# Performance work log

Hardware: AMD Instinct MI355X
Metric: run time of the kernel (lower is better)

## Reference

```python
import jax, jax.numpy as jnp
import numpy as np


def lstm_cell(x, h, c, Wi, Wh, b):
    # PyTorch LSTMCell gate order: i, f, g, o
    g = x @ Wi.T + h @ Wh.T + b
    i, f, gg, o = jnp.split(g, 4, axis=-1)
    c = jax.nn.sigmoid(f) * c + jax.nn.sigmoid(i) * jnp.tanh(gg)
    h = jax.nn.sigmoid(o) * jnp.tanh(c)
    return h, c


def setup_inputs() -> dict:
    key = jax.random.key(0)
    ks = jax.random.split(key, 32)
    S, B, L, N, T = 20, 16, 30, 6, 20
    H, E, Vs, Vt = 512, 512, 50000, 30000
    w = lambda k, shape: jax.random.normal(k, shape, jnp.float32) * 0.05
    return {
        'articles': jax.random.randint(ks[0], (S, B, L), 0, Vs, jnp.int32),
        'summaries': jax.random.randint(ks[1], (N, B, T), 0, Vt, jnp.int32),
        'emb_src': w(ks[2], (Vs, E)),
        'emb_tgt': w(ks[3], (Vt, E)),
        'we_Wi': w(ks[4], (4 * H, E)), 'we_Wh': w(ks[5], (4 * H, H)), 'we_b': w(ks[6], (4 * H,)),
        'se_Wi': w(ks[7], (4 * H, H)), 'se_Wh': w(ks[8], (4 * H, H)), 'se_b': w(ks[9], (4 * H,)),
        'W_feat': w(ks[10], (H, H)), 'b_feat': w(ks[11], (H,)),
        'wd_Wi': w(ks[12], (4 * H, E)), 'wd_Wh': w(ks[13], (4 * H, H)), 'wd_b': w(ks[14], (4 * H,)),
        'W_vocab': w(ks[15], (Vt, H)), 'b_vocab': w(ks[16], (Vt,)),
        'sd_Wi': w(ks[17], (4 * H, H)), 'sd_Wh': w(ks[18], (4 * H, H)), 'sd_b': w(ks[19], (4 * H,)),
        'attn_Wh': w(ks[20], (H, H)), 'attn_wc': w(ks[21], (H,)), 'attn_v': w(ks[22], (H,)),
        'W_out': w(ks[23], (H, 2 * H)), 'b_out': w(ks[24], (H,)),
    }


def _forward(articles, summaries, emb_src, emb_tgt, we_Wi, we_Wh, we_b,
             se_Wi, se_Wh, se_b, W_feat, b_feat, wd_Wi, wd_Wh, wd_b,
             W_vocab, b_vocab, sd_Wi, sd_Wh, sd_b, attn_Wh, attn_wc, attn_v,
             W_out, b_out):
    S, B, L = articles.shape
    H = we_Wh.shape[1]

    # ---- word encoder: LSTMCell over each sentence, vmapped over S ----
    def encode_sentence(tokens):  # [B, L]
        x = emb_src[tokens]  # [B, L, E]
        z = jnp.zeros((B, H), x.dtype)
        def step(hc, xt):
            h, c = lstm_cell(xt, hc[0], hc[1], we_Wi, we_Wh, we_b)
            return (h, c), None
        (h, _), _ = jax.lax.scan(step, (z, z), jnp.swapaxes(x, 0, 1))
        return h
    word_hx = jax.vmap(encode_sentence)(articles)  # [S, B, H]

    # ---- sentence encoder: LSTM over sentence dim ----
    z = jnp.zeros((B, H), word_hx.dtype)
    def senc_step(hc, x):
        h, c = lstm_cell(x, hc[0], hc[1], se_Wi, se_Wh, se_b)
        return (h, c), h
    (s_hx, s_cx), sent_out = jax.lax.scan(senc_step, (z, z), word_hx)  # sent_out [S,B,H]
    sent_feat = sent_out @ W_feat.T + b_feat  # precomputed attention features

    mask = (articles[:, :, 0:1] > 0).astype(jnp.float32)  # [S, B, 1]
    coverage0 = jnp.zeros_like(mask)

    # ---- hierarchical decoder over summary sentences ----
    def sent_step(carry, sent):  # sent [B, T]
        w_hx, w_cx, s_hx, s_cx, coverage, loss = carry
        seq = sent.T  # [T, B]

        def word_step(wc, ba):
            wh, wcell, l = wc
            wb, wa = ba
            wh, wcell = lstm_cell(emb_tgt[wb], wh, wcell, wd_Wi, wd_Wh, wd_b)
            logits = wh @ W_vocab.T + b_vocab  # [B, V]
            logp = jax.nn.log_softmax(logits, axis=-1)
            nll = -jnp.take_along_axis(logp, wa[:, None], axis=1)[:, 0]
            m = (wa != 0).astype(logits.dtype)  # ignore_index=0
            l = l + jnp.sum(nll * m) / jnp.maximum(jnp.sum(m), 1.0)
            return (wh, wcell, l), None

        (w_hx, w_cx, loss), _ = jax.lax.scan(word_step, (w_hx, w_cx, loss), (seq[:-1], seq[1:]))

        # sentence decoder step with coverage attention over S sentences
        s_h2, s_cx = lstm_cell(w_hx, s_hx, s_cx, sd_Wi, sd_Wh, sd_b)
        e = jnp.einsum('sbh,h->sb', jnp.tanh(sent_feat + s_h2 @ attn_Wh.T + coverage * attn_wc), attn_v)
        e = jnp.where(mask[:, :, 0] > 0, e, -1e9)
        align = jax.nn.softmax(e, axis=0)[:, :, None]  # [S, B, 1]
        context = jnp.sum(align * sent_out, axis=0)  # [B, H]
        final = jnp.tanh(jnp.concatenate([context, s_h2], axis=-1) @ W_out.T + b_out)
        # coverage loss (with pre-update coverage), then accumulate coverage
        loss = loss + jnp.mean(jnp.sum(jnp.minimum(align[:, :, 0], coverage[:, :, 0]), axis=0))
        coverage = coverage + align
        return (final, w_cx, final, s_cx, coverage, loss), None

    init = (s_hx, s_cx, s_hx, s_cx, coverage0, jnp.float32(0.0))
    (_, _, _, _, _, loss), _ = jax.lax.scan(sent_step, init, summaries)
    return loss


def reference(articles, summaries, emb_src, emb_tgt, we_Wi, we_Wh, we_b,
              se_Wi, se_Wh, se_b, W_feat, b_feat, wd_Wi, wd_Wh, wd_b,
              W_vocab, b_vocab, sd_Wi, sd_Wh, sd_b, attn_Wh, attn_wc, attn_v,
              W_out, b_out):
    return _forward(articles, summaries, emb_src, emb_tgt, we_Wi, we_Wh, we_b,
                    se_Wi, se_Wh, se_b, W_feat, b_feat, wd_Wi, wd_Wh, wd_b,
                    W_vocab, b_vocab, sd_Wi, sd_Wh, sd_b, attn_Wh, attn_wc,
                    attn_v, W_out, b_out)
```

## Files before the change

kernel.cpp:

```cpp
#include <hip/hip_runtime.h>
#include <cstdint>
#include <cstddef>

#define H 512
#define SS 20
#define BB 16
#define LL 30
#define NN 6
#define TT 20
#define VT 30000
#define MROWS 1824
#define NSTEPS 114
#define MPAD 1856
#define NT2 120
#define VBLK 232
#define UBLK 16

typedef __attribute__((ext_vector_type(8))) short bf16x8;
typedef __attribute__((ext_vector_type(4))) float f32x4;

__device__ __forceinline__ float sigmoidf_(float x) { return 1.f / (1.f + expf(-x)); }
__device__ __forceinline__ float b2f(ushort u) { return __uint_as_float(((uint32_t)u) << 16); }
__device__ __forceinline__ ushort f2b_rne(float f) {
  uint32_t u = __float_as_uint(f);
  return (ushort)((u + 0x7fffu + ((u >> 16) & 1u)) >> 16);
}

__device__ __forceinline__ void gbar(uint* cnt, uint* gen, uint nblk)
{
  __syncthreads();
  if (threadIdx.x == 0) {
    uint g = __hip_atomic_load(gen, __ATOMIC_RELAXED, __HIP_MEMORY_SCOPE_AGENT);
    uint v = __hip_atomic_fetch_add(cnt, 1u, __ATOMIC_ACQ_REL, __HIP_MEMORY_SCOPE_AGENT);
    if (v == nblk - 1u) {
      __hip_atomic_store(cnt, 0u, __ATOMIC_RELAXED, __HIP_MEMORY_SCOPE_AGENT);
      __hip_atomic_store(gen, g + 1u, __ATOMIC_RELEASE, __HIP_MEMORY_SCOPE_AGENT);
    } else {
      while (__hip_atomic_load(gen, __ATOMIC_ACQUIRE, __HIP_MEMORY_SCOPE_AGENT) == g)
        __builtin_amdgcn_s_sleep(2);
    }
  }
  __syncthreads();
}

struct PrepP {
  const int* articles; const int* summaries;
  const float* emb_src; const float* emb_tgt;
  const float* we_Wi; const float* wd_Wi; const float* we_Wh;
  const float* se_Wi; const float* se_Wh; const float* W_feat;
  const float* wd_Wh; const float* sd_Wi; const float* sd_Wh;
  const float* attn_Wh; const float* W_out;
  ushort* A_we; ushort* A_wd;
  ushort* weWi; ushort* wdWi; ushort* weWh;
  ushort* seWi; ushort* seWh; ushort* wfeat;
  ushort* wdWh; ushort* sdWi; ushort* sdWh;
  ushort* attnWh; ushort* Wout;
};

__device__ __forceinline__ void conv_f2b(const float* __restrict__ src,
                                         ushort* __restrict__ dst, int n4,
                                         int t0, int stride)
{
  for (int i = t0; i < n4; i += stride) {
    float4 v = reinterpret_cast<const float4*>(src)[i];
    ushort4 o;
    o.x = f2b_rne(v.x); o.y = f2b_rne(v.y);
    o.z = f2b_rne(v.z); o.w = f2b_rne(v.w);
    reinterpret_cast<ushort4*>(dst)[i] = o;
  }
}

__global__ __launch_bounds__(256) void prep_kernel(PrepP P)
{
  const int t0 = blockIdx.x * 256 + threadIdx.x;
  const int stride = gridDim.x * 256;
  for (int i = t0; i < SS * BB * LL * H; i += stride) {
    int m = i >> 9, k = i & 511;
    int l = m / (SS * BB), sb = m % (SS * BB);
    int tok = P.articles[sb * LL + l];
    P.A_we[i] = f2b_rne(P.emb_src[(size_t)tok * H + k]);
  }
  for (int i = t0; i < MROWS * H; i += stride) {
    int m = i >> 9, k = i & 511;
    int stp = m >> 4, b = m & 15;
    int n = stp / (TT - 1), t = stp % (TT - 1);
    int tok = P.summaries[(n * BB + b) * TT + t];
    P.A_wd[i] = f2b_rne(P.emb_tgt[(size_t)tok * H + k]);
  }
  const int Q = 4 * H * H / 4;
  conv_f2b(P.we_Wi, P.weWi, Q, t0, stride);
  conv_f2b(P.wd_Wi, P.wdWi, Q, t0, stride);
  conv_f2b(P.we_Wh, P.weWh, Q, t0, stride);
  conv_f2b(P.se_Wi, P.seWi, Q, t0, stride);
  conv_f2b(P.se_Wh, P.seWh, Q, t0, stride);
  conv_f2b(P.wd_Wh, P.wdWh, Q, t0, stride);
  conv_f2b(P.sd_Wi, P.sdWi, Q, t0, stride);
  conv_f2b(P.sd_Wh, P.sdWh, Q, t0, stride);
  conv_f2b(P.W_feat, P.wfeat, H * H / 4, t0, stride);
  conv_f2b(P.attn_Wh, P.attnWh, H * H / 4, t0, stride);
  conv_f2b(P.W_out, P.Wout, H * 2 * H / 4, t0, stride);
}

__global__ __launch_bounds__(512) void proj_mfma_kernel(
    const ushort* __restrict__ A_we, const ushort* __restrict__ weWi,
    const float* __restrict__ we_b, ushort* __restrict__ XiW,
    const ushort* __restrict__ A_wd, const ushort* __restrict__ wdWi,
    const float* __restrict__ wd_b, ushort* __restrict__ XiD)
{
  int bid = blockIdx.x;
  const ushort* A; const ushort* W; const float* bias; ushort* C; int M, mt, nt;
  if (bid < 1200) { A = A_we; W = weWi; bias = we_b; C = XiW; M = 9600; mt = bid >> 3; nt = bid & 7; }
  else { int b2 = bid - 1200; A = A_wd; W = wdWi; bias = wd_b; C = XiD; M = MROWS; mt = b2 >> 3; nt = b2 & 7; }
  const int tid = threadIdx.x, wid = tid >> 6, lane = tid & 63;
  const int wm = wid >> 2, wn = wid & 3;
  const int m0 = mt * 64 + wm * 32, n0 = nt * 256 + wn * 64;
  const int lr = lane & 15, lk = (lane >> 4) << 3;

  f32x4 acc[2][4];
#pragma unroll
  for (int i = 0; i < 2; ++i)
#pragma unroll
    for (int nf = 0; nf < 4; ++nf) acc[i][nf] = (f32x4)0.0f;

  for (int k0 = 0; k0 < H; k0 += 32) {
    bf16x8 a[2], b[4];
#pragma unroll
    for (int i = 0; i < 2; ++i) {
      int m = m0 + i * 16 + lr;
      bf16x8 az = (bf16x8)(short)0;
      if (m < M) az = *reinterpret_cast<const bf16x8*>(A + (size_t)m * H + k0 + lk);
      a[i] = az;
    }
#pragma unroll
    for (int nf = 0; nf < 4; ++nf)
      b[nf] = *reinterpret_cast<const bf16x8*>(W + (size_t)(n0 + nf * 16 + lr) * H + k0 + lk);
#pragma unroll
    for (int i = 0; i < 2; ++i)
#pragma unroll
      for (int nf = 0; nf < 4; ++nf)
        acc[i][nf] = __builtin_amdgcn_mfma_f32_16x16x32_bf16(a[i], b[nf], acc[i][nf], 0, 0, 0);
  }
#pragma unroll
  for (int i = 0; i < 2; ++i)
#pragma unroll
    for (int nf = 0; nf < 4; ++nf) {
      int n = n0 + nf * 16 + lr;
      float bv = bias[n];
#pragma unroll
      for (int jreg = 0; jreg < 4; ++jreg) {
        int row = m0 + i * 16 + (lane >> 4) * 4 + jreg;
        if (row < M) C[(size_t)row * 2048 + n] = f2b_rne(acc[i][nf][jreg] + bv);
      }
    }
}

struct UP {
  const ushort* XiW; const ushort* XiD;
  const ushort* weWh; const ushort* seWi; const ushort* seWh;
  const ushort* wfeat; const ushort* wdWh; const ushort* sdWi;
  const ushort* sdWh; const ushort* attnWh; const ushort* Wout;
  const float* se_b; const float* b_feat; const float* sd_b; const float* b_out;
  const float* attn_wc; const float* attn_v; const int* articles;
  ushort* h0; ushort* h1;
  float* XiS;
  ushort* sh0; ushort* sh1;
  float* sent_out; ushort* sent_out_bf; float* sent_feat;
  ushort* wh_bf; ushort* sdh_bf; ushort* final_bf; ushort* catb;
  float* qb; float* ebuf; float* alignb; float* covb; float* loss;
  uint* bcnt; uint* bgen;
};

__global__ __launch_bounds__(512) void uni_kernel(UP P)
{
  __shared__ f32x4 hred[2][4][64];
  const int tid = threadIdx.x, bid = blockIdx.x;
  const int wid = tid >> 6, lane = tid & 63;
  const int gw = bid * 8 + wid;
  const int lr = lane & 15;
  const int lk = (lane >> 4) << 3;
  const int orow = (lane >> 4) << 2;

  {
    float cst[5][4];
#pragma unroll
    for (int it = 0; it < 5; ++it)
#pragma unroll
      for (int rg = 0; rg < 4; ++rg) cst[it][rg] = 0.f;
    ushort* cur = P.h0;
    ushort* nxt = P.h1;
    const int ug = gw & 31;
    const int unit = ug * 16 + lr;
    const ushort* wb = P.weWh + (size_t)(ug * 16 + lr) * H + lk;
    for (int l = 0; l < LL; ++l) {
#pragma unroll
      for (int it = 0; it < 5; ++it) {
        int item = gw + it * 128;
        int mt = item >> 5;
        f32x4 acc[4];
#pragma unroll
        for (int g = 0; g < 4; ++g) acc[g] = (f32x4)0.0f;
        const ushort* ab = cur + (size_t)(mt * 16 + lr) * H + lk;
#pragma unroll
        for (int k0 = 0; k0 < H; k0 += 32) {
          bf16x8 a = *reinterpret_cast<const bf16x8*>(ab + k0);
#pragma unroll
          for (int g = 0; g < 4; ++g) {
            bf16x8 b = *reinterpret_cast<const bf16x8*>(wb + (size_t)g * H * H + k0);
            acc[g] = __builtin_amdgcn_mfma_f32_16x16x32_bf16(a, b, acc[g], 0, 0, 0);
          }
        }
#pragma unroll
        for (int rg = 0; rg < 4; ++rg) {
          int row = mt * 16 + orow + rg;
          const ushort* xi = P.XiW + (size_t)(l * 320 + row) * 2048 + unit;
          float gi = acc[0][rg] + b2f(xi[0]);
          float gf = acc[1][rg] + b2f(xi[512]);
          float gc = acc[2][rg] + b2f(xi[1024]);
          float go = acc[3][rg] + b2f(xi[1536]);
          float c = sigmoidf_(gf) * cst[it][rg] + sigmoidf_(gi) * tanhf(gc);
          float h = sigmoidf_(go) * tanhf(c);
          cst[it][rg] = c;
          nxt[(size_t)row * H + unit] = f2b_rne(h);
        }
      }
      gbar(P.bcnt, P.bgen, UBLK);
      ushort* t = cur; cur = nxt; nxt = t;
    }
    {
      const ushort* wbs = P.seWi + (size_t)(ug * 16 + lr) * H + lk;
#pragma unroll
      for (int it = 0; it < 5; ++it) {
        int item = gw + it * 128;
        int mt = item >> 5;
        f32x4 acc[4];
#pragma unroll
        for (int g = 0; g < 4; ++g) acc[g] = (f32x4)0.0f;
        const ushort* ab = cur + (size_t)(mt * 16 + lr) * H + lk;
#pragma unroll
        for (int k0 = 0; k0 < H; k0 += 32) {
          bf16x8 a = *reinterpret_cast<const bf16x8*>(ab + k0);
#pragma unroll
          for (int g = 0; g < 4; ++g) {
            bf16x8 b = *reinterpret_cast<const bf16x8*>(wbs + (size_t)g * H * H + k0);
            acc[g] = __builtin_amdgcn_mfma_f32_16x16x32_bf16(a, b, acc[g], 0, 0, 0);
          }
        }
#pragma unroll
        for (int rg = 0; rg < 4; ++rg) {
          int row = mt * 16 + orow + rg;
#pragma unroll
          for (int g = 0; g < 4; ++g)
            P.XiS[(size_t)row * 2048 + g * H + unit] = acc[g][rg] + P.se_b[g * H + unit];
        }
      }
    }
    gbar(P.bcnt, P.bgen, UBLK);
  }

  float cw[4] = {0.f, 0.f, 0.f, 0.f};
  float csd[4] = {0.f, 0.f, 0.f, 0.f};
  {
    float cse[4] = {0.f, 0.f, 0.f, 0.f};
    ushort* cur = P.sh0;
    ushort* nxt = P.sh1;
    const int ug = bid * 2 + wid;
    const int unit = ug * 16 + lr;
    for (int s = 0; s < SS; ++s) {
      if (wid < 2) {
        f32x4 acc[4];
#pragma unroll
        for (int g = 0; g < 4; ++g) acc[g] = (f32x4)0.0f;
        const ushort* ab = cur + (size_t)lr * H + lk;
        const ushort* wb = P.seWh + (size_t)(ug * 16 + lr) * H + lk;
#pragma unroll
        for (int k0 = 0; k0 < H; k0 += 32) {
          bf16x8 a = *reinterpret_cast<const bf16x8*>(ab + k0);
#pragma unroll
          for (int g = 0; g < 4; ++g) {
            bf16x8 b = *reinterpret_cast<const bf16x8*>(wb + (size_t)g * H * H + k0);
            acc[g] = __builtin_amdgcn_mfma_f32_16x16x32_bf16(a, b, acc[g], 0, 0, 0);
          }
        }
#pragma unroll
        for (int rg = 0; rg < 4; ++rg) {
          int row = orow + rg;
          const float* xi = P.XiS + (size_t)(s * 16 + row) * 2048 + unit;
          float gi = acc[0][rg] + xi[0];
          float gf = acc[1][rg] + xi[512];
          float gc = acc[2][rg] + xi[1024];
          float go = acc[3][rg] + xi[1536];
          float c = sigmoidf_(gf) * cse[rg] + sigmoidf_(gi) * tanhf(gc);
          float h = sigmoidf_(go) * tanhf(c);
          cse[rg] = c;
          nxt[(size_t)row * H + unit] = f2b_rne(h);
          P.sent_out[(size_t)(s * 16 + row) * H + unit] = h;
          P.sent_out_bf[(size_t)(s * 16 + row) * H + unit] = f2b_rne(h);
        }
      }
      gbar(P.bcnt, P.bgen, UBLK);
      ushort* t = cur; cur = nxt; nxt = t;
    }
    if (wid < 2) {
      f32x4 v; v[0] = cse[0]; v[1] = cse[1]; v[2] = cse[2]; v[3] = cse[3];
      hred[wid][0][lane] = v;
#pragma unroll
      for (int rg = 0; rg < 4; ++rg) csd[rg] = cse[rg];
    }
    __syncthreads();
    if (wid < 4 && !(wid & 1)) {
      f32x4 v = hred[wid >> 1][0][lane];
      cw[0] = v[0]; cw[1] = v[1]; cw[2] = v[2]; cw[3] = v[3];
    }
    __syncthreads();
  }

  {
    const int ug = gw & 31;
    const int unit = ug * 16 + lr;
    const ushort* wb = P.wfeat + (size_t)(ug * 16 + lr) * H + lk;
#pragma unroll
    for (int it = 0; it < 5; ++it) {
      int item = gw + it * 128;
      int mt = item >> 5;
      f32x4 acc = (f32x4)0.0f;
      const ushort* ab = P.sent_out_bf + (size_t)(mt * 16 + lr) * H + lk;
#pragma unroll
      for (int k0 = 0; k0 < H; k0 += 32) {
        bf16x8 a = *reinterpret_cast<const bf16x8*>(ab + k0);
        bf16x8 b = *reinterpret_cast<const bf16x8*>(wb + k0);
        acc = __builtin_amdgcn_mfma_f32_16x16x32_bf16(a, b, acc, 0, 0, 0);
      }
#pragma unroll
      for (int rg = 0; rg < 4; ++rg) {
        int row = mt * 16 + orow + rg;
        P.sent_feat[(size_t)row * H + unit] = acc[rg] + P.b_feat[unit];
      }
    }
    gbar(P.bcnt, P.bgen, UBLK);
  }

  {
    const int half = wid & 1;
    const int ug2 = bid * 2 + (wid >> 1);
    const int unit2 = ug2 * 16 + lr;
    const int ug = bid * 2 + wid;
    const int unit = ug * 16 + lr;

    for (int n = 0; n < NN; ++n) {
      bf16x8 wreg[4][8];
      if (wid < 4) {
#pragma unroll
        for (int g = 0; g < 4; ++g)
#pragma unroll
          for (int kk = 0; kk < 8; ++kk)
            wreg[g][kk] = *reinterpret_cast<const bf16x8*>(
                P.wdWh + (size_t)g * H * H + (size_t)(ug2 * 16 + lr) * H +
                half * 256 + kk * 32 + lk);
      }
      for (int t = 0; t < TT - 1; ++t) {
        int stp = n * (TT - 1) + t;
        f32x4 acc[4];
        if (wid < 4) {
          const ushort* A = (t == 0)
              ? ((n == 0) ? P.sh0 : P.final_bf)
              : P.wh_bf + (size_t)(stp - 1) * 16 * H;
#pragma unroll
          for (int g = 0; g < 4; ++g) acc[g] = (f32x4)0.0f;
          const ushort* ab = A + (size_t)lr * H + half * 256 + lk;
#pragma unroll
          for (int kk = 0; kk < 8; ++kk) {
            bf16x8 a = *reinterpret_cast<const bf16x8*>(ab + kk * 32);
#pragma unroll
            for (int g = 0; g < 4; ++g)
              acc[g] = __builtin_amdgcn_mfma_f32_16x16x32_bf16(a, wreg[g][kk], acc[g], 0, 0, 0);
          }
          if (half) {
#pragma unroll
            for (int g = 0; g < 4; ++g) hred[wid >> 1][g][lane] = acc[g];
          }
        }
        __syncthreads();
        if (wid < 4 && !half) {
#pragma unroll
          for (int g = 0; g < 4; ++g) {
            f32x4 o = hred[wid >> 1][g][lane];
            acc[g] += o;
          }
#pragma unroll
          for (int rg = 0; rg < 4; ++rg) {
            int row = orow + rg;
            const ushort* xi = P.XiD + (size_t)(stp * 16 + row) * 2048 + unit2;
            float gi = acc[0][rg] + b2f(xi[0]);
            float gf = acc[1][rg] + b2f(xi[512]);
            float gc = acc[2][rg] + b2f(xi[1024]);
            float go = acc[3][rg] + b2f(xi[1536]);
            float c = sigmoidf_(gf) * cw[rg] + sigmoidf_(gi) * tanhf(gc);
            float h = sigmoidf_(go) * tanhf(c);
            cw[rg] = c;
            P.wh_bf[(size_t)(stp * 16 + row) * H + unit2] = f2b_rne(h);
          }
        }
        gbar(P.bcnt, P.bgen, UBLK);
      }
      if (wid < 2) {
        f32x4 acc[4];
#pragma unroll
        for (int g = 0; g < 4; ++g) acc[g] = (f32x4)0.0f;
        const ushort* A1 = P.wh_bf + (size_t)(n * (TT - 1) + TT - 2) * 16 * H;
        const ushort* A2 = (n == 0) ? P.sh0 : P.final_bf;
        const ushort* ab1 = A1 + (size_t)lr * H + lk;
        const ushort* wb1 = P.sdWi + (size_t)(ug * 16 + lr) * H + lk;
#pragma unroll
        for (int k0 = 0; k0 < H; k0 += 32) {
          bf16x8 a = *reinterpret_cast<const bf16x8*>(ab1 + k0);
#pragma unroll
          for (int g = 0; g < 4; ++g) {
            bf16x8 b = *reinterpret_cast<const bf16x8*>(wb1 + (size_t)g * H * H + k0);
            acc[g] = __builtin_amdgcn_mfma_f32_16x16x32_bf16(a, b, acc[g], 0, 0, 0);
          }
        }
        const ushort* ab2 = A2 + (size_t)lr * H + lk;
        const ushort* wb2 = P.sdWh + (size_t)(ug * 16 + lr) * H + lk;
#pragma unroll
        for (int k0 = 0; k0 < H; k0 += 32) {
          bf16x8 a = *reinterpret_cast<const bf16x8*>(ab2 + k0);
#pragma unroll
          for (int g = 0; g < 4; ++g) {
            bf16x8 b = *reinterpret_cast<const bf16x8*>(wb2 + (size_t)g * H * H + k0);
            acc[g] = __builtin_amdgcn_mfma_f32_16x16x32_bf16(a, b, acc[g], 0, 0, 0);
          }
        }
#pragma unroll
        for (int rg = 0; rg < 4; ++rg) {
          int row = orow + rg;
          float gi = acc[0][rg] + P.sd_b[0 * H + unit];
          float gf = acc[1][rg] + P.sd_b[1 * H + unit];
          float gc = acc[2][rg] + P.sd_b[2 * H + unit];
          float go = acc[3][rg] + P.sd_b[3 * H + unit];
          float c = sigmoidf_(gf) * csd[rg] + sigmoidf_(gi) * tanhf(gc);
          float h = sigmoidf_(go) * tanhf(c);
          csd[rg] = c;
          P.sdh_bf[(size_t)row * H + unit] = f2b_rne(h);
        }
      }
      gbar(P.bcnt, P.bgen, UBLK);
      if (wid < 2) {
        f32x4 acc = (f32x4)0.0f;
        const ushort* ab = P.sdh_bf + (size_t)lr * H + lk;
        const ushort* wb = P.attnWh + (size_t)(ug * 16 + lr) * H + lk;
#pragma unroll
        for (int k0 = 0; k0 < H; k0 += 32) {
          bf16x8 a = *reinterpret_cast<const bf16x8*>(ab + k0);
          bf16x8 b = *reinterpret_cast<const bf16x8*>(wb + k0);
          acc = __builtin_amdgcn_mfma_f32_16x16x32_bf16(a, b, acc, 0, 0, 0);
        }
#pragma unroll
        for (int rg = 0; rg < 4; ++rg)
          P.qb[(size_t)(orow + rg) * H + unit] = acc[rg];
      }
      gbar(P.bcnt, P.bgen, UBLK);
      for (int sb = gw; sb < 320; sb += 128) {
        int b = sb & 15;
        float cov = P.covb[sb];
        float sum = 0.f;
        for (int h2 = lane; h2 < H; h2 += 64)
          sum += tanhf(P.sent_feat[(size_t)sb * H + h2] + P.qb[b * H + h2] +
                       cov * P.attn_wc[h2]) * P.attn_v[h2];
#pragma unroll
        for (int d = 1; d < 64; d <<= 1) sum += __shfl_xor(sum, d);
        if (lane == 0)
          P.ebuf[sb] = (P.articles[sb * LL] > 0) ? sum : -1e9f;
      }
      gbar(P.bcnt, P.bgen, UBLK);
      if (wid == 0) {
        int b = bid;
        float ev = (lane < SS) ? P.ebuf[lane * 16 + b] : -3.0e38f;
        float mx = ev;
#pragma unroll
        for (int d = 1; d < 64; d <<= 1) mx = fmaxf(mx, __shfl_xor(mx, d));
        float ex = (lane < SS) ? expf(ev - mx) : 0.f;
        float s = ex;
#pragma unroll
        for (int d = 1; d < 64; d <<= 1) s += __shfl_xor(s, d);
        float al = ex / s;
        float cl = 0.f;
        if (lane < SS) {
          int sb = lane * 16 + b;
          float cov = P.covb[sb];
          cl = fminf(al, cov);
          P.covb[sb] = cov + al;
          P.alignb[sb] = al;
        }
#pragma unroll
        for (int d = 1; d < 64; d <<= 1) cl += __shfl_xor(cl, d);
        if (lane == 0) atomicAdd(P.loss, cl * (1.f / BB));
      }
      gbar(P.bcnt, P.bgen, UBLK);
      {
        int idx = bid * 512 + tid;
        int b = idx >> 9, h2 = idx & 511;
        float s = 0.f;
#pragma unroll
        for (int ss2 = 0; ss2 < SS; ++ss2)
          s += P.alignb[ss2 * 16 + b] * P.sent_out[(size_t)(ss2 * 16 + b) * H + h2];
        P.catb[b * 1024 + h2] = f2b_rne(s);
        P.catb[b * 1024 + 512 + h2] = P.sdh_bf[(size_t)b * H + h2];
      }
      gbar(P.bcnt, P.bgen, UBLK);
      if (wid < 2) {
        f32x4 acc = (f32x4)0.0f;
        const ushort* ab = P.catb + (size_t)lr * 1024 + lk;
        const ushort* wb = P.Wout + (size_t)(ug * 16 + lr) * 1024 + lk;
#pragma unroll
        for (int k0 = 0; k0 < 1024; k0 += 32) {
          bf16x8 a = *reinterpret_cast<const bf16x8*>(ab + k0);
          bf16x8 b = *reinterpret_cast<const bf16x8*>(wb + k0);
          acc = __builtin_amdgcn_mfma_f32_16x16x32_bf16(a, b, acc, 0, 0, 0);
        }
#pragma unroll
        for (int rg = 0; rg < 4; ++rg) {
          int row = orow + rg;
          float v = tanhf(acc[rg] + P.b_out[unit]);
          P.final_bf[(size_t)row * H + unit] = f2b_rne(v);
        }
      }
      gbar(P.bcnt, P.bgen, UBLK);
    }
  }
}

__global__ __launch_bounds__(512) void vocab_kernel(
    const ushort* __restrict__ A, const float* __restrict__ Wf,
    ushort* __restrict__ Wbf, const float* __restrict__ bias,
    float* __restrict__ partials, uint* bcnt, uint* bgen)
{
  {
    int t0 = blockIdx.x * 512 + threadIdx.x;
    const int n4 = VT * H / 4;
    for (int i = t0; i < n4; i += VBLK * 512) {
      float4 v = reinterpret_cast<const float4*>(Wf)[i];
      ushort4 o;
      o.x = f2b_rne(v.x); o.y = f2b_rne(v.y);
      o.z = f2b_rne(v.z); o.w = f2b_rne(v.w);
      reinterpret_cast<ushort4*>(Wbf)[i] = o;
    }
  }
  gbar(bcnt, bgen, VBLK);

  __shared__ float red[4][64][2];
  const int bid = blockIdx.x;
  const int chunk = bid & 7, mt = bid >> 3;
  const int tid = threadIdx.x;
  const int wid = tid >> 6, lane = tid & 63;
  const int wm = wid >> 2, wn = wid & 3;
  const int m0 = mt * 64 + wm * 32;
  const int lr = lane & 15;
  const int lk = (lane >> 4) << 3;

  bf16x8 areg[2][16];
#pragma unroll
  for (int i = 0; i < 2; ++i)
#pragma unroll
    for (int kk = 0; kk < 16; ++kk)
      areg[i][kk] = *reinterpret_cast<const bf16x8*>(
          A + (size_t)(m0 + i * 16 + lr) * H + kk * 32 + lk);

  for (int nt2 = 0; nt2 < 15; ++nt2) {
    const int n0 = chunk * 3840 + nt2 * 256 + wn * 64;
    f32x4 acc[2][4];
#pragma unroll
    for (int i = 0; i < 2; ++i)
#pragma unroll
      for (int nf = 0; nf < 4; ++nf) acc[i][nf] = (f32x4)0.0f;

#pragma unroll 4
    for (int kk = 0; kk < 16; ++kk) {
      bf16x8 b[4];
#pragma unroll
      for (int nf = 0; nf < 4; ++nf) {
        int n = n0 + nf * 16 + lr;
        bf16x8 bz = (bf16x8)(short)0;
        if (n < VT) bz = *reinterpret_cast<const bf16x8*>(Wbf + (size_t)n * H + kk * 32 + lk);
        b[nf] = bz;
      }
#pragma unroll
      for (int i = 0; i < 2; ++i)
#pragma unroll
        for (int nf = 0; nf < 4; ++nf)
          acc[i][nf] = __builtin_amdgcn_mfma_f32_16x16x32_bf16(areg[i][kk], b[nf], acc[i][nf], 0, 0, 0);
    }

    float bc[4];
    int val[4];
#pragma unroll
    for (int nf = 0; nf < 4; ++nf) {
      int n = n0 + nf * 16 + lr;
      val[nf] = (n < VT);
      bc[nf] = val[nf] ? bias[n] : 0.f;
    }
#pragma unroll
    for (int i = 0; i < 2; ++i) {
#pragma unroll
      for (int jreg = 0; jreg < 4; ++jreg) {
        float lg[4];
        float mx = -3.0e38f;
#pragma unroll
        for (int nf = 0; nf < 4; ++nf) {
          lg[nf] = val[nf] ? (acc[i][nf][jreg] + bc[nf]) : -3.0e38f;
          mx = fmaxf(mx, lg[nf]);
        }
#pragma unroll
        for (int d = 1; d < 16; d <<= 1) mx = fmaxf(mx, __shfl_xor(mx, d));
        float s = 0.f;
#pragma unroll
        for (int nf = 0; nf < 4; ++nf) s += val[nf] ? expf(lg[nf] - mx) : 0.f;
#pragma unroll
        for (int d = 1; d < 16; d <<= 1) s += __shfl_xor(s, d);
        if (lr == 0) {
          int rloc = wm * 32 + i * 16 + (lane >> 4) * 4 + jreg;
          red[wn][rloc][0] = mx;
          red[wn][rloc][1] = s;
        }
      }
    }
    __syncthreads();
    if (tid < 64) {
      int r2 = tid;
      float M = -3.0e38f;
#pragma unroll
      for (int w = 0; w < 4; ++w) M = fmaxf(M, red[w][r2][0]);
      float S = 0.f;
#pragma unroll
      for (int w = 0; w < 4; ++w) S += red[w][r2][1] * expf(red[w][r2][0] - M);
      size_t p = ((size_t)(mt * 64 + r2) * NT2 + chunk * 15 + nt2) * 2;
      partials[p] = M;
      partials[p + 1] = S;
    }
    __syncthreads();
  }
}

__global__ void tlog_kernel(const ushort* __restrict__ wh_bf,
                            const ushort* __restrict__ Wv_bf,
                            const float* __restrict__ bv,
                            const int* __restrict__ summaries,
                            float* __restrict__ tlog)
{
  int row = blockIdx.x;
  int lane = threadIdx.x;
  int b = row & 15, stp = row >> 4;
  int n = stp / (TT - 1), t = stp % (TT - 1);
  int tgt = summaries[(n * BB + b) * TT + t + 1];
  float s = 0.f;
  for (int k = lane; k < H; k += 64)
    s += b2f(wh_bf[(size_t)row * H + k]) * b2f(Wv_bf[(size_t)tgt * H + k]);
#pragma unroll
  for (int d = 1; d < 64; d <<= 1) s += __shfl_xor(s, d);
  if (lane == 0) tlog[row] = s + bv[tgt];
}

__global__ __launch_bounds__(256) void nll_kernel(
    const float* __restrict__ partials, const float* __restrict__ tlog,
    const int* __restrict__ summaries, float* __restrict__ loss)
{
  int stp = blockIdx.x;
  int tid = threadIdx.x;
  int rr = tid >> 4, ch = tid & 15;
  int row = stp * 16 + rr;
  const float* pr = partials + (size_t)row * NT2 * 2;
  float mx = -3.0e38f;
  for (int t2 = ch; t2 < NT2; t2 += 16) mx = fmaxf(mx, pr[t2 * 2]);
#pragma unroll
  for (int d = 1; d < 16; d <<= 1) mx = fmaxf(mx, __shfl_xor(mx, d));
  float s = 0.f;
  for (int t2 = ch; t2 < NT2; t2 += 16) s += pr[t2 * 2 + 1] * expf(pr[t2 * 2] - mx);
#pragma unroll
  for (int d = 1; d < 16; d <<= 1) s += __shfl_xor(s, d);
  __shared__ float sh_n[16], sh_m[16];
  if (ch == 0) {
    float lse = mx + logf(s);
    float nll = lse - tlog[row];
    int b = row & 15;
    int n = stp / (TT - 1), t = stp % (TT - 1);
    int wa = summaries[(n * BB + b) * TT + t + 1];
    sh_n[rr] = (wa != 0) ? nll : 0.f;
    sh_m[rr] = (wa != 0) ? 1.f : 0.f;
  }
  __syncthreads();
  if (tid == 0) {
    float sn = 0.f, sm = 0.f;
    for (int r2 = 0; r2 < 16; ++r2) { sn += sh_n[r2]; sm += sh_m[r2]; }
    atomicAdd(loss, sn / fmaxf(sm, 1.f));
  }
}

extern "C" void kernel_launch(void* const* d_in, const int* in_sizes, int n_in,
                              void* d_out, int out_size, void* d_ws, size_t ws_size,
                              hipStream_t stream)
{
  (void)in_sizes; (void)n_in; (void)out_size; (void)ws_size;
  const int*   articles  = (const int*)d_in[0];
  const int*   summaries = (const int*)d_in[1];
  const float* emb_src   = (const float*)d_in[2];
  const float* emb_tgt   = (const float*)d_in[3];
  const float* we_Wi = (const float*)d_in[4];
  const float* we_Wh = (const float*)d_in[5];
  const float* we_b  = (const float*)d_in[6];
  const float* se_Wi = (const float*)d_in[7];
  const float* se_Wh = (const float*)d_in[8];
  const float* se_b  = (const float*)d_in[9];
  const float* W_feat = (const float*)d_in[10];
  const float* b_feat = (const float*)d_in[11];
  const float* wd_Wi = (const float*)d_in[12];
  const float* wd_Wh = (const float*)d_in[13];
  const float* wd_b  = (const float*)d_in[14];
  const float* W_vocab = (const float*)d_in[15];
  const float* b_vocab = (const float*)d_in[16];
  const float* sd_Wi = (const float*)d_in[17];
  const float* sd_Wh = (const float*)d_in[18];
  const float* sd_b  = (const float*)d_in[19];
  const float* attn_Wh = (const float*)d_in[20];
  const float* attn_wc = (const float*)d_in[21];
  const float* attn_v  = (const float*)d_in[22];
  const float* W_out = (const float*)d_in[23];
  const float* b_out = (const float*)d_in[24];

  char* wsb = (char*)d_ws;
  size_t off = 0;
  auto alloc = [&](size_t bytes) -> char* {
    char* p = wsb + off;
    off += (bytes + 255) & ~(size_t)255;
    return p;
  };

  char* regA = alloc(9830400);
  ushort* A_we     = (ushort*)regA;
  ushort* wh_bf    = (ushort*)regA;
  float*  partials = (float*)(regA + 1900544);
  float*  tlogb    = (float*)(regA + 3682304);

  ushort* A_wd = (ushort*)alloc((size_t)MROWS * H * 2);

  char* regW = alloc((size_t)9600 * 2048 * 2);
  ushort* XiW   = (ushort*)regW;
  ushort* Wv_bf = (ushort*)regW;

  ushort* XiD = (ushort*)alloc((size_t)MROWS * 2048 * 2);

  ushort* weWi  = (ushort*)alloc(4 * H * H * 2);
  ushort* wdWi  = (ushort*)alloc(4 * H * H * 2);
  ushort* weWh  = (ushort*)alloc(4 * H * H * 2);
  ushort* seWi  = (ushort*)alloc(4 * H * H * 2);
  ushort* seWh  = (ushort*)alloc(4 * H * H * 2);
  ushort* wdWh  = (ushort*)alloc(4 * H * H * 2);
  ushort* sdWi  = (ushort*)alloc(4 * H * H * 2);
  ushort* sdWh  = (ushort*)alloc(4 * H * H * 2);
  ushort* wfeat = (ushort*)alloc(H * H * 2);
  ushort* attnWh= (ushort*)alloc(H * H * 2);
  ushort* Wout  = (ushort*)alloc(H * 2 * H * 2);

  float*  XiS = (float*)alloc((size_t)320 * 2048 * 4);
  ushort* h0  = (ushort*)alloc(320 * H * 2);
  ushort* h1  = (ushort*)alloc(320 * H * 2);
  ushort* sh0 = (ushort*)alloc(16 * H * 2);
  ushort* sh1 = (ushort*)alloc(16 * H * 2);
  float*  sent_out    = (float*)alloc(320 * H * 4);
  ushort* sent_out_bf = (ushort*)alloc(320 * H * 2);
  float*  sent_feat   = (float*)alloc(320 * H * 4);
  ushort* sdh_bf   = (ushort*)alloc(16 * H * 2);
  ushort* final_bf = (ushort*)alloc(16 * H * 2);
  ushort* catb     = (ushort*)alloc(16 * 1024 * 2);
  float*  qb       = (float*)alloc(16 * H * 4);
  float*  ebuf   = (float*)alloc(1280);
  float*  alignb = (float*)alloc(1280);
  float*  covb   = (float*)alloc(1280);
  uint*   bar    = (uint*)alloc(256);

  float* loss = (float*)d_out;
  hipMemsetAsync(loss, 0, 4, stream);
  hipMemsetAsync(covb, 0, 1280, stream);
  hipMemsetAsync(h0, 0, 320 * H * 2, stream);
  hipMemsetAsync(sh0, 0, 16 * H * 2, stream);
  hipMemsetAsync(bar, 0, 256, stream);

  {
    PrepP P = {articles, summaries, emb_src, emb_tgt,
               we_Wi, wd_Wi, we_Wh, se_Wi, se_Wh, W_feat,
               wd_Wh, sd_Wi, sd_Wh, attn_Wh, W_out,
               A_we, A_wd, weWi, wdWi, weWh, seWi, seWh, wfeat,
               wdWh, sdWi, sdWh, attnWh, Wout};
    prep_kernel<<<2048, 256, 0, stream>>>(P);
  }

  proj_mfma_kernel<<<1432, 512, 0, stream>>>(A_we, weWi, we_b, XiW,
                                             A_wd, wdWi, wd_b, XiD);

  hipMemsetAsync((char*)wh_bf + (size_t)MROWS * H * 2, 0,
                 (size_t)(MPAD - MROWS) * H * 2, stream);

  {
    UP P;
    P.XiW = XiW; P.XiD = XiD;
    P.weWh = weWh; P.seWi = seWi; P.seWh = seWh; P.wfeat = wfeat;
    P.wdWh = wdWh; P.sdWi = sdWi; P.sdWh = sdWh; P.attnWh = attnWh; P.Wout = Wout;
    P.se_b = se_b; P.b_feat = b_feat; P.sd_b = sd_b; P.b_out = b_out;
    P.attn_wc = attn_wc; P.attn_v = attn_v; P.articles = articles;
    P.h0 = h0; P.h1 = h1; P.XiS = XiS; P.sh0 = sh0; P.sh1 = sh1;
    P.sent_out = sent_out; P.sent_out_bf = sent_out_bf; P.sent_feat = sent_feat;
    P.wh_bf = wh_bf; P.sdh_bf = sdh_bf; P.final_bf = final_bf; P.catb = catb;
    P.qb = qb; P.ebuf = ebuf; P.alignb = alignb; P.covb = covb; P.loss = loss;
    P.bcnt = bar; P.bgen = bar + 1;
    uni_kernel<<<UBLK, 512, 0, stream>>>(P);
  }

  vocab_kernel<<<VBLK, 512, 0, stream>>>(wh_bf, W_vocab, Wv_bf, b_vocab,
                                         partials, bar + 2, bar + 3);
  tlog_kernel<<<MROWS, 64, 0, stream>>>(wh_bf, Wv_bf, b_vocab, summaries, tlogb);
  nll_kernel<<<NSTEPS, 256, 0, stream>>>(partials, tlogb, summaries, loss);
}
```

Before: 5.198 ms.

## Replace counter grid barrier with per-block flag barrier and relaxed atomic data exchange

The persistent recurrent kernel's grid barrier moves from a centralized atomic counter plus generation scheme to per-block phase flags. Each block publishes its phase and polls all peers. All data shared across blocks now travels through relaxed agent-scope atomic loads and stores, with bf16 outputs packed in pairs via lane shuffles. The aim is to cut the latency of the many per-step barriers, which take acquire/release fences. The trade-off is that memory ordering now rests on relaxed atomics with no explicit fences, and scattered atomic accesses may cost more bandwidth than plain vector loads.

```diff
diff --git a/kernel.cpp b/kernel.cpp
--- a/kernel.cpp
+++ b/kernel.cpp
@@ -16,6 +16,8 @@
 #define VBLK 232
 #define UBLK 16
 
+#define SCOPE_AGENT __HIP_MEMORY_SCOPE_AGENT
+
 typedef __attribute__((ext_vector_type(8))) short bf16x8;
 typedef __attribute__((ext_vector_type(4))) float f32x4;
 
@@ -26,17 +28,54 @@
   return (ushort)((u + 0x7fffu + ((u >> 16) & 1u)) >> 16);
 }
 
+__device__ __forceinline__ void ast_u32(uint* p, uint v) {
+  __hip_atomic_store(p, v, __ATOMIC_RELAXED, SCOPE_AGENT);
+}
+__device__ __forceinline__ uint ald_u32(const uint* p) {
+  return __hip_atomic_load(p, __ATOMIC_RELAXED, SCOPE_AGENT);
+}
+__device__ __forceinline__ void ast_f32(float* p, float v) {
+  __hip_atomic_store(p, v, __ATOMIC_RELAXED, SCOPE_AGENT);
+}
+__device__ __forceinline__ float ald_f32(const float* p) {
+  return __hip_atomic_load(p, __ATOMIC_RELAXED, SCOPE_AGENT);
+}
+union BF8U { unsigned long long u[2]; bf16x8 v; };
+__device__ __forceinline__ bf16x8 ald_bf8(const ushort* p) {
+  const unsigned long long* q = (const unsigned long long*)p;
+  BF8U r;
+  r.u[0] = __hip_atomic_load(q,     __ATOMIC_RELAXED, SCOPE_AGENT);
+  r.u[1] = __hip_atomic_load(q + 1, __ATOMIC_RELAXED, SCOPE_AGENT);
+  return r.v;
+}
+__device__ __forceinline__ void ast_pair(ushort* addr_even, ushort myv, int lane) {
+  uint other = __shfl_xor((uint)myv, 1);
+  if (!(lane & 1)) ast_u32((uint*)addr_even, (uint)myv | (other << 16));
+}
+
+__device__ __forceinline__ void fbar(uint* flags, int bid, int nblk, uint phase)
+{
+  __syncthreads();
+  if (threadIdx.x == 0)
+    ast_u32(&flags[bid * 16], phase);
+  if ((int)threadIdx.x < nblk) {
+    while (ald_u32(&flags[threadIdx.x * 16]) < phase)
+      __builtin_amdgcn_s_sleep(1);
+  }
+  __syncthreads();
+}
+
 __device__ __forceinline__ void gbar(uint* cnt, uint* gen, uint nblk)
 {
   __syncthreads();
   if (threadIdx.x == 0) {
-    uint g = __hip_atomic_load(gen, __ATOMIC_RELAXED, __HIP_MEMORY_SCOPE_AGENT);
-    uint v = __hip_atomic_fetch_add(cnt, 1u, __ATOMIC_ACQ_REL, __HIP_MEMORY_SCOPE_AGENT);
+    uint g = __hip_atomic_load(gen, __ATOMIC_RELAXED, SCOPE_AGENT);
+    uint v = __hip_atomic_fetch_add(cnt, 1u, __ATOMIC_ACQ_REL, SCOPE_AGENT);
     if (v == nblk - 1u) {
-      __hip_atomic_store(cnt, 0u, __ATOMIC_RELAXED, __HIP_MEMORY_SCOPE_AGENT);
-      __hip_atomic_store(gen, g + 1u, __ATOMIC_RELEASE, __HIP_MEMORY_SCOPE_AGENT);
+      __hip_atomic_store(cnt, 0u, __ATOMIC_RELAXED, SCOPE_AGENT);
+      __hip_atomic_store(gen, g + 1u, __ATOMIC_RELEASE, SCOPE_AGENT);
     } else {
-      while (__hip_atomic_load(gen, __ATOMIC_ACQUIRE, __HIP_MEMORY_SCOPE_AGENT) == g)
+      while (__hip_atomic_load(gen, __ATOMIC_ACQUIRE, SCOPE_AGENT) == g)
         __builtin_amdgcn_s_sleep(2);
     }
   }
@@ -167,7 +206,7 @@
   float* sent_out; ushort* sent_out_bf; float* sent_feat;
   ushort* wh_bf; ushort* sdh_bf; ushort* final_bf; ushort* catb;
   float* qb; float* ebuf; float* alignb; float* covb; float* loss;
-  uint* bcnt; uint* bgen;
+  uint* flags;
 };
 
 __global__ __launch_bounds__(512) void uni_kernel(UP P)
@@ -179,6 +218,7 @@
   const int lr = lane & 15;
   const int lk = (lane >> 4) << 3;
   const int orow = (lane >> 4) << 2;
+  uint ph = 0;
 
   {
     float cst[5][4];
@@ -194,15 +234,14 @@
     for (int l = 0; l < LL; ++l) {
 #pragma unroll
       for (int it = 0; it < 5; ++it) {
-        int item = gw + it * 128;
-        int mt = item >> 5;
+        int mt = (gw + it * 128) >> 5;
         f32x4 acc[4];
 #pragma unroll
         for (int g = 0; g < 4; ++g) acc[g] = (f32x4)0.0f;
         const ushort* ab = cur + (size_t)(mt * 16 + lr) * H + lk;
 #pragma unroll
         for (int k0 = 0; k0 < H; k0 += 32) {
-          bf16x8 a = *reinterpret_cast<const bf16x8*>(ab + k0);
+          bf16x8 a = ald_bf8(ab + k0);
 #pragma unroll
           for (int g = 0; g < 4; ++g) {
             bf16x8 b = *reinterpret_cast<const bf16x8*>(wb + (size_t)g * H * H + k0);
@@ -220,25 +259,24 @@
           float c = sigmoidf_(gf) * cst[it][rg] + sigmoidf_(gi) * tanhf(gc);
           float h = sigmoidf_(go) * tanhf(c);
           cst[it][rg] = c;
-          nxt[(size_t)row * H + unit] = f2b_rne(h);
-        }
-      }
-      gbar(P.bcnt, P.bgen, UBLK);
+          ast_pair(nxt + (size_t)row * H + (unit & ~1), f2b_rne(h), lane);
+        }
+      }
+      fbar(P.flags, bid, UBLK, ++ph);
       ushort* t = cur; cur = nxt; nxt = t;
     }
     {
       const ushort* wbs = P.seWi + (size_t)(ug * 16 + lr) * H + lk;
 #pragma unroll
       for (int it = 0; it < 5; ++it) {
-        int item = gw + it * 128;
-        int mt = item >> 5;
+        int mt = (gw + it * 128) >> 5;
         f32x4 acc[4];
 #pragma unroll
         for (int g = 0; g < 4; ++g) acc[g] = (f32x4)0.0f;
         const ushort* ab = cur + (size_t)(mt * 16 + lr) * H + lk;
 #pragma unroll
         for (int k0 = 0; k0 < H; k0 += 32) {
-          bf16x8 a = *reinterpret_cast<const bf16x8*>(ab + k0);
+          bf16x8 a = ald_bf8(ab + k0);
 #pragma unroll
           for (int g = 0; g < 4; ++g) {
             bf16x8 b = *reinterpret_cast<const bf16x8*>(wbs + (size_t)g * H * H + k0);
@@ -250,11 +288,12 @@
           int row = mt * 16 + orow + rg;
 #pragma unroll
           for (int g = 0; g < 4; ++g)
-            P.XiS[(size_t)row * 2048 + g * H + unit] = acc[g][rg] + P.se_b[g * H + unit];
-        }
-      }
-    }
-    gbar(P.bcnt, P.bgen, UBLK);
+            ast_f32(&P.XiS[(size_t)row * 2048 + g * H + unit],
+                    acc[g][rg] + P.se_b[g * H + unit]);
+        }
+      }
+    }
+    fbar(P.flags, bid, UBLK, ++ph);
   }
 
   float cw[4] = {0.f, 0.f, 0.f, 0.f};
@@ -274,7 +313,7 @@
         const ushort* wb = P.seWh + (size_t)(ug * 16 + lr) * H + lk;
 #pragma unroll
         for (int k0 = 0; k0 < H; k0 += 32) {
-          bf16x8 a = *reinterpret_cast<const bf16x8*>(ab + k0);
+          bf16x8 a = ald_bf8(ab + k0);
 #pragma unroll
           for (int g = 0; g < 4; ++g) {
             bf16x8 b = *reinterpret_cast<const bf16x8*>(wb + (size_t)g * H * H + k0);
@@ -284,20 +323,24 @@
 #pragma unroll
         for (int rg = 0; rg < 4; ++rg) {
           int row = orow + rg;
-          const float* xi = P.XiS + (size_t)(s * 16 + row) * 2048 + unit;
-          float gi = acc[0][rg] + xi[0];
-          float gf = acc[1][rg] + xi[512];
-          float gc = acc[2][rg] + xi[1024];
-          float go = acc[3][rg] + xi[1536];
+          float gi = acc[0][rg] + ald_f32(&P.XiS[(size_t)(s * 16 + row) * 2048 + 0 * H + unit]);
+          float gf = acc[1][rg] + ald_f32(&P.XiS[(size_t)(s * 16 + row) * 2048 + 1 * H + unit]);
+          float gc = acc[2][rg] + ald_f32(&P.XiS[(size_t)(s * 16 + row) * 2048 + 2 * H + unit]);
+          float go = acc[3][rg] + ald_f32(&P.XiS[(size_t)(s * 16 + row) * 2048 + 3 * H + unit]);
           float c = sigmoidf_(gf) * cse[rg] + sigmoidf_(gi) * tanhf(gc);
           float h = sigmoidf_(go) * tanhf(c);
           cse[rg] = c;
-          nxt[(size_t)row * H + unit] = f2b_rne(h);
-          P.sent_out[(size_t)(s * 16 + row) * H + unit] = h;
-          P.sent_out_bf[(size_t)(s * 16 + row) * H + unit] = f2b_rne(h);
-        }
-      }
-      gbar(P.bcnt, P.bgen, UBLK);
+          ushort hv = f2b_rne(h);
+          uint other = __shfl_xor((uint)hv, 1);
+          if (!(lane & 1)) {
+            uint pk = (uint)hv | (other << 16);
+            ast_u32((uint*)(nxt + (size_t)row * H + (unit & ~1)), pk);
+            ast_u32((uint*)(P.sent_out_bf + (size_t)(s * 16 + row) * H + (unit & ~1)), pk);
+          }
+          ast_f32(&P.sent_out[(size_t)(s * 16 + row) * H + unit], h);
+        }
+      }
+      fbar(P.flags, bid, UBLK, ++ph);
       ushort* t = cur; cur = nxt; nxt = t;
     }
     if (wid < 2) {
@@ -320,23 +363,22 @@
     const ushort* wb = P.wfeat + (size_t)(ug * 16 + lr) * H + lk;
 #pragma unroll
     for (int it = 0; it < 5; ++it) {
-      int item = gw + it * 128;
-      int mt = item >> 5;
+      int mt = (gw + it * 128) >> 5;
       f32x4 acc = (f32x4)0.0f;
       const ushort* ab = P.sent_out_bf + (size_t)(mt * 16 + lr) * H + lk;
 #pragma unroll
       for (int k0 = 0; k0 < H; k0 += 32) {
-        bf16x8 a = *reinterpret_cast<const bf16x8*>(ab + k0);
+        bf16x8 a = ald_bf8(ab + k0);
         bf16x8 b = *reinterpret_cast<const bf16x8*>(wb + k0);
         acc = __builtin_amdgcn_mfma_f32_16x16x32_bf16(a, b, acc, 0, 0, 0);
       }
 #pragma unroll
       for (int rg = 0; rg < 4; ++rg) {
         int row = mt * 16 + orow + rg;
-        P.sent_feat[(size_t)row * H + unit] = acc[rg] + P.b_feat[unit];
-      }
-    }
-    gbar(P.bcnt, P.bgen, UBLK);
+        ast_f32(&P.sent_feat[(size_t)row * H + unit], acc[rg] + P.b_feat[unit]);
+      }
+    }
+    fbar(P.flags, bid, UBLK, ++ph);
   }
 
   {
@@ -369,7 +411,7 @@
           const ushort* ab = A + (size_t)lr * H + half * 256 + lk;
 #pragma unroll
           for (int kk = 0; kk < 8; ++kk) {
-            bf16x8 a = *reinterpret_cast<const bf16x8*>(ab + kk * 32);
+            bf16x8 a = ald_bf8(ab + kk * 32);
 #pragma unroll
             for (int g = 0; g < 4; ++g)
               acc[g] = __builtin_amdgcn_mfma_f32_16x16x32_bf16(a, wreg[g][kk], acc[g], 0, 0, 0);
@@ -382,10 +424,7 @@
         __syncthreads();
         if (wid < 4 && !half) {
 #pragma unroll
-          for (int g = 0; g < 4; ++g) {
-            f32x4 o = hred[wid >> 1][g][lane];
-            acc[g] += o;
-          }
+          for (int g = 0; g < 4; ++g) acc[g] += hred[wid >> 1][g][lane];
 #pragma unroll
           for (int rg = 0; rg < 4; ++rg) {
             int row = orow + rg;
@@ -397,10 +436,11 @@
             float c = sigmoidf_(gf) * cw[rg] + sigmoidf_(gi) * tanhf(gc);
             float h = sigmoidf_(go) * tanhf(c);
             cw[rg] = c;
-            P.wh_bf[(size_t)(stp * 16 + row) * H + unit2] = f2b_rne(h);
+            ast_pair(P.wh_bf + (size_t)(stp * 16 + row) * H + (unit2 & ~1),
+                     f2b_rne(h), lane);
           }
         }
-        gbar(P.bcnt, P.bgen, UBLK);
+        fbar(P.flags, bid, UBLK, ++ph);
       }
       if (wid < 2) {
         f32x4 acc[4];
@@ -412,7 +452,7 @@
         const ushort* wb1 = P.sdWi + (size_t)(ug * 16 + lr) * H + lk;
 #pragma unroll
         for (int k0 = 0; k0 < H; k0 += 32) {
-          bf16x8 a = *reinterpret_cast<const bf16x8*>(ab1 + k0);
+          bf16x8 a = ald_bf8(ab1 + k0);
 #pragma unroll
           for (int g = 0; g < 4; ++g) {
             bf16x8 b = *reinterpret_cast<const bf16x8*>(wb1 + (size_t)g * H * H + k0);
@@ -423,7 +463,7 @@
         const ushort* wb2 = P.sdWh + (size_t)(ug * 16 + lr) * H + lk;
 #pragma unroll
         for (int k0 = 0; k0 < H; k0 += 32) {
-          bf16x8 a = *reinterpret_cast<const bf16x8*>(ab2 + k0);
+          bf16x8 a = ald_bf8(ab2 + k0);
 #pragma unroll
           for (int g = 0; g < 4; ++g) {
             bf16x8 b = *reinterpret_cast<const bf16x8*>(wb2 + (size_t)g * H * H + k0);
@@ -440,41 +480,42 @@
           float c = sigmoidf_(gf) * csd[rg] + sigmoidf_(gi) * tanhf(gc);
           float h = sigmoidf_(go) * tanhf(c);
           csd[rg] = c;
-          P.sdh_bf[(size_t)row * H + unit] = f2b_rne(h);
-        }
-      }
-      gbar(P.bcnt, P.bgen, UBLK);
+          ast_pair(P.sdh_bf + (size_t)row * H + (unit & ~1), f2b_rne(h), lane);
+        }
+      }
+      fbar(P.flags, bid, UBLK, ++ph);
       if (wid < 2) {
         f32x4 acc = (f32x4)0.0f;
         const ushort* ab = P.sdh_bf + (size_t)lr * H + lk;
         const ushort* wb = P.attnWh + (size_t)(ug * 16 + lr) * H + lk;
 #pragma unroll
         for (int k0 = 0; k0 < H; k0 += 32) {
-          bf16x8 a = *reinterpret_cast<const bf16x8*>(ab + k0);
+          bf16x8 a = ald_bf8(ab + k0);
           bf16x8 b = *reinterpret_cast<const bf16x8*>(wb + k0);
           acc = __builtin_amdgcn_mfma_f32_16x16x32_bf16(a, b, acc, 0, 0, 0);
         }
 #pragma unroll
         for (int rg = 0; rg < 4; ++rg)
-          P.qb[(size_t)(orow + rg) * H + unit] = acc[rg];
-      }
-      gbar(P.bcnt, P.bgen, UBLK);
+          ast_f32(&P.qb[(size_t)(orow + rg) * H + unit], acc[rg]);
+      }
+      fbar(P.flags, bid, UBLK, ++ph);
       for (int sb = gw; sb < 320; sb += 128) {
         int b = sb & 15;
-        float cov = P.covb[sb];
+        float cov = ald_f32(&P.covb[sb]);
         float sum = 0.f;
         for (int h2 = lane; h2 < H; h2 += 64)
-          sum += tanhf(P.sent_feat[(size_t)sb * H + h2] + P.qb[b * H + h2] +
+          sum += tanhf(ald_f32(&P.sent_feat[(size_t)sb * H + h2]) +
+                       ald_f32(&P.qb[b * H + h2]) +
                        cov * P.attn_wc[h2]) * P.attn_v[h2];
 #pragma unroll
         for (int d = 1; d < 64; d <<= 1) sum += __shfl_xor(sum, d);
         if (lane == 0)
-          P.ebuf[sb] = (P.articles[sb * LL] > 0) ? sum : -1e9f;
-      }
-      gbar(P.bcnt, P.bgen, UBLK);
+          ast_f32(&P.ebuf[sb], (P.articles[sb * LL] > 0) ? sum : -1e9f);
+      }
+      fbar(P.flags, bid, UBLK, ++ph);
       if (wid == 0) {
         int b = bid;
-        float ev = (lane < SS) ? P.ebuf[lane * 16 + b] : -3.0e38f;
+        float ev = (lane < SS) ? ald_f32(&P.ebuf[lane * 16 + b]) : -3.0e38f;
         float mx = ev;
 #pragma unroll
         for (int d = 1; d < 64; d <<= 1) mx = fmaxf(mx, __shfl_xor(mx, d));
@@ -486,34 +527,40 @@
         float cl = 0.f;
         if (lane < SS) {
           int sb = lane * 16 + b;
-          float cov = P.covb[sb];
+          float cov = ald_f32(&P.covb[sb]);
           cl = fminf(al, cov);
-          P.covb[sb] = cov + al;
-          P.alignb[sb] = al;
+          ast_f32(&P.covb[sb], cov + al);
+          ast_f32(&P.alignb[sb], al);
         }
 #pragma unroll
         for (int d = 1; d < 64; d <<= 1) cl += __shfl_xor(cl, d);
         if (lane == 0) atomicAdd(P.loss, cl * (1.f / BB));
       }
-      gbar(P.bcnt, P.bgen, UBLK);
+      fbar(P.flags, bid, UBLK, ++ph);
       {
         int idx = bid * 512 + tid;
         int b = idx >> 9, h2 = idx & 511;
         float s = 0.f;
 #pragma unroll
         for (int ss2 = 0; ss2 < SS; ++ss2)
-          s += P.alignb[ss2 * 16 + b] * P.sent_out[(size_t)(ss2 * 16 + b) * H + h2];
-        P.catb[b * 1024 + h2] = f2b_rne(s);
-        P.catb[b * 1024 + 512 + h2] = P.sdh_bf[(size_t)b * H + h2];
-      }
-      gbar(P.bcnt, P.bgen, UBLK);
+          s += ald_f32(&P.alignb[ss2 * 16 + b]) *
+               ald_f32(&P.sent_out[(size_t)(ss2 * 16 + b) * H + h2]);
+        ushort sv = f2b_rne(s);
+        uint other = __shfl_xor((uint)sv, 1);
+        if (!(lane & 1)) {
+          ast_u32((uint*)(P.catb + (size_t)b * 1024 + h2), (uint)sv | (other << 16));
+          uint sd2 = ald_u32((const uint*)(P.sdh_bf + (size_t)b * H + h2));
+          ast_u32((uint*)(P.catb + (size_t)b * 1024 + 512 + h2), sd2);
+        }
+      }
+      fbar(P.flags, bid, UBLK, ++ph);
       if (wid < 2) {
         f32x4 acc = (f32x4)0.0f;
         const ushort* ab = P.catb + (size_t)lr * 1024 + lk;
         const ushort* wb = P.Wout + (size_t)(ug * 16 + lr) * 1024 + lk;
 #pragma unroll
         for (int k0 = 0; k0 < 1024; k0 += 32) {
-          bf16x8 a = *reinterpret_cast<const bf16x8*>(ab + k0);
+          bf16x8 a = ald_bf8(ab + k0);
           bf16x8 b = *reinterpret_cast<const bf16x8*>(wb + k0);
           acc = __builtin_amdgcn_mfma_f32_16x16x32_bf16(a, b, acc, 0, 0, 0);
         }
@@ -521,10 +568,10 @@
         for (int rg = 0; rg < 4; ++rg) {
           int row = orow + rg;
           float v = tanhf(acc[rg] + P.b_out[unit]);
-          P.final_bf[(size_t)row * H + unit] = f2b_rne(v);
-        }
-      }
-      gbar(P.bcnt, P.bgen, UBLK);
+          ast_pair(P.final_bf + (size_t)row * H + (unit & ~1), f2b_rne(v), lane);
+        }
+      }
+      fbar(P.flags, bid, UBLK, ++ph);
     }
   }
 }
@@ -775,6 +822,7 @@
   float*  alignb = (float*)alloc(1280);
   float*  covb   = (float*)alloc(1280);
   uint*   bar    = (uint*)alloc(256);
+  uint*   flags  = (uint*)alloc(UBLK * 16 * 4);
 
   float* loss = (float*)d_out;
   hipMemsetAsync(loss, 0, 4, stream);
@@ -782,6 +830,7 @@
   hipMemsetAsync(h0, 0, 320 * H * 2, stream);
   hipMemsetAsync(sh0, 0, 16 * H * 2, stream);
   hipMemsetAsync(bar, 0, 256, stream);
+  hipMemsetAsync(flags, 0, UBLK * 16 * 4, stream);
 
   {
     PrepP P = {articles, summaries, emb_src, emb_tgt,
@@ -809,12 +858,12 @@
     P.sent_out = sent_out; P.sent_out_bf = sent_out_bf; P.sent_feat = sent_feat;
     P.wh_bf = wh_bf; P.sdh_bf = sdh_bf; P.final_bf = final_bf; P.catb = catb;
     P.qb = qb; P.ebuf = ebuf; P.alignb = alignb; P.covb = covb; P.loss = loss;
-    P.bcnt = bar; P.bgen = bar + 1;
+    P.flags = flags;
     uni_kernel<<<UBLK, 512, 0, stream>>>(P);
   }
 
   vocab_kernel<<<VBLK, 512, 0, stream>>>(wh_bf, W_vocab, Wv_bf, b_vocab,
-                                         partials, bar + 2, bar + 3);
+                                         partials, bar, bar + 1);
   tlog_kernel<<<MROWS, 64, 0, stream>>>(wh_bf, Wv_bf, b_vocab, summaries, tlogb);
   nll_kernel<<<NSTEPS, 256, 0, stream>>>(partials, tlogb, summaries, loss);
 }
```

After: 5.726 ms. 1.1x slower.
